# Kernel optimization log

Hardware: AMD Instinct MI355X
Metric: run time of the kernel (lower is better)

Reference implementation:

```python
import jax, jax.numpy as jnp
import numpy as np

B, S, H = 2, 2048, 2048
NQ, NKV = 32, 8          # query heads, kv heads
G = NQ // NKV            # query groups per kv head
D = H // NQ              # head dim = 64
MAX_POS = 4096
THETA = 10000.0


def _rope_tables(position_ids):
    # freqs per the original apply_rotary_emb (interleaved pair convention)
    freqs = 1.0 / THETA ** (jnp.arange(0, D, 2)[: D // 2].astype(jnp.float32) / D)
    t = jnp.arange(MAX_POS, dtype=jnp.float32)
    ang = jnp.outer(t, freqs)                     # [MAX_POS, D/2]
    cos = jnp.take(jnp.cos(ang), position_ids, axis=0)[:, :, None, :]  # [B,S,1,D/2]
    sin = jnp.take(jnp.sin(ang), position_ids, axis=0)[:, :, None, :]
    return cos, sin


def _apply_rope(x, cos, sin):
    # x: [B,S,h,D]; pairs are interleaved (x0,x1),(x2,x3),...
    x2 = x.astype(jnp.float32).reshape(*x.shape[:-1], D // 2, 2)
    xr, xi = x2[..., 0], x2[..., 1]
    out_r = xr * cos - xi * sin
    out_i = xr * sin + xi * cos
    return jnp.stack((out_r, out_i), axis=-1).reshape(x.shape).astype(x.dtype)


def setup_inputs() -> dict:
    key = jax.random.key(0)
    ks = jax.random.split(key, 5)
    init_scale = 0.02 / np.sqrt(H)
    hidden_states = jax.random.normal(ks[0], (B, S, H), dtype=jnp.float32)
    wq = jax.random.normal(ks[1], (H, H), dtype=jnp.float32) * init_scale
    wk = jax.random.normal(ks[2], (H, H // G), dtype=jnp.float32) * init_scale
    wv = jax.random.normal(ks[3], (H, H // G), dtype=jnp.float32) * init_scale
    wo = jax.random.normal(ks[4], (H, H), dtype=jnp.float32) * init_scale
    attention_mask = jnp.ones((B, S), dtype=jnp.int32)
    position_ids = jnp.broadcast_to(jnp.arange(S, dtype=jnp.int32), (B, S))
    return dict(hidden_states=hidden_states, attention_mask=attention_mask,
                position_ids=position_ids, wq=wq, wk=wk, wv=wv, wo=wo)


def reference(hidden_states, attention_mask, position_ids, wq, wk, wv, wo):
    # projections (no bias)
    xq = (hidden_states @ wq).reshape(B, S, NQ, D)
    xk = (hidden_states @ wk).reshape(B, S, NKV, D)
    xv = (hidden_states @ wv).reshape(B, S, NKV, D)
    # GQA repeat: kv head h -> query heads h*G .. h*G+G-1 (consecutive)
    xk = jnp.repeat(xk, G, axis=2)  # [B,S,NQ,D]
    xv = jnp.repeat(xv, G, axis=2)

    cos, sin = _rope_tables(position_ids)
    xq = _apply_rope(xq, cos, sin)
    xk = _apply_rope(xk, cos, sin)

    # causal + padding mask -> additive bias
    causal = jnp.tril(jnp.ones((S, S), dtype=bool))[None, None]          # [1,1,S,S]
    pad = (attention_mask > 0)[:, None, None, :]                          # [B,1,1,S]
    combined = jnp.logical_and(causal, pad)                               # [B,1,S,S]
    neg = jnp.finfo(jnp.float32).min
    bias = jnp.where(combined, 0.0, neg).astype(jnp.float32)

    scale = 1.0 / np.sqrt(D)
    scores = jnp.einsum('bqhd,bkhd->bhqk', xq, xk).astype(jnp.float32) * scale
    scores = scores + bias
    attn = jax.nn.softmax(scores, axis=-1)                                # [B,NQ,S,S] fp32
    out = jnp.einsum('bhqk,bkhd->bqhd', attn, xv)                         # [B,S,NQ,D]
    out = out.reshape(B, S, H)
    return out @ wo
```

## Files before the change

### kernel.cpp

```cpp
#include <hip/hip_runtime.h>
#include <cstdint>

typedef __attribute__((ext_vector_type(8))) __bf16  bf8v;
typedef __attribute__((ext_vector_type(4))) float   f4v;
typedef __attribute__((ext_vector_type(4))) short   s4v;
typedef __attribute__((ext_vector_type(8))) unsigned short ush8;

__device__ __forceinline__ float bf2f(unsigned short u) {
    union { unsigned u; float f; } v; v.u = ((unsigned)u) << 16; return v.f;
}
__device__ __forceinline__ unsigned short f2bf_n(float f) {
    union { __bf16 h; unsigned short s; } v; v.h = (__bf16)f; return v.s;
}
__device__ __forceinline__ unsigned pack2bf(float a, float b) {
    union { __bf16 h[2]; unsigned u; } v;
    v.h[0] = (__bf16)a; v.h[1] = (__bf16)b; return v.u;
}

#define GLDS16(gp, lp)                                                          \
    __builtin_amdgcn_global_load_lds(                                           \
        (const __attribute__((address_space(1))) void*)(uintptr_t)(gp),         \
        (__attribute__((address_space(3))) void*)(uintptr_t)(lp), 16, 0, 0)

__global__ void cast_f32_to_bf16(const float* __restrict__ in,
                                 unsigned short* __restrict__ out, int n8) {
    int i = blockIdx.x * 256 + threadIdx.x;
    if (i >= n8) return;
    float4 a = ((const float4*)in)[2 * i];
    float4 b = ((const float4*)in)[2 * i + 1];
    uint4 o;
    o.x = pack2bf(a.x, a.y);
    o.y = pack2bf(a.z, a.w);
    o.z = pack2bf(b.x, b.y);
    o.w = pack2bf(b.z, b.w);
    ((uint4*)out)[i] = o;
}

__global__ void transpose_cast(const float* __restrict__ in,
                               unsigned short* __restrict__ out, int R, int C) {
    __shared__ float t[32][33];
    int c0 = blockIdx.x * 32, r0 = blockIdx.y * 32;
    int x = threadIdx.x, y = threadIdx.y;
    #pragma unroll
    for (int i = 0; i < 32; i += 8) t[y + i][x] = in[(size_t)(r0 + y + i) * C + c0 + x];
    __syncthreads();
    #pragma unroll
    for (int i = 0; i < 32; i += 8)
        out[(size_t)(c0 + y + i) * R + r0 + x] = f2bf_n(t[x][y + i]);
}

__global__ void transpose_v_bf16(const unsigned short* __restrict__ in,
                                 unsigned short* __restrict__ out) {
    __shared__ unsigned short t[32][33];
    int c0 = blockIdx.x * 32;
    int r0 = blockIdx.y * 32;
    int x = threadIdx.x, y = threadIdx.y;
    #pragma unroll
    for (int i = 0; i < 32; i += 8)
        t[y + i][x] = in[(size_t)(r0 + y + i) * 3072 + 2560 + c0 + x];
    __syncthreads();
    #pragma unroll
    for (int i = 0; i < 32; i += 8) {
        int d   = c0 + y + i;
        int tok = r0 + x;
        int g   = (tok >> 2) & 15;
        int tp  = (tok & ~63) | (((g ^ (d & 15)) << 2)) | (tok & 3);
        out[(size_t)d * 4096 + tp] = t[x][y + i];
    }
}

__global__ void rope_strided(unsigned short* __restrict__ X,
                             const int* __restrict__ pos_ids,
                             int coloff, int stride, int nh_log2) {
    int idx = blockIdx.x * 256 + threadIdx.x;
    int i   = idx & 31;
    int hh  = (idx >> 5) & ((1 << nh_log2) - 1);
    int tok = idx >> (5 + nh_log2);
    int pos = pos_ids[tok];
    float ang = (float)pos * exp2f(-0.41524101186092f * (float)i);
    float s = sinf(ang), c = cosf(ang);
    unsigned short* p = X + (size_t)tok * stride + coloff + hh * 64 + 2 * i;
    unsigned pr = *(const unsigned*)p;
    float xr = bf2f((unsigned short)(pr & 0xffff));
    float xi = bf2f((unsigned short)(pr >> 16));
    float orr = xr * c - xi * s;
    float oi  = xr * s + xi * c;
    *(unsigned*)p = pack2bf(orr, oi);
}

template <int OUT_BF16>
__global__ __launch_bounds__(256) void gemm_bt(const unsigned short* __restrict__ A,
                                               const unsigned short* __restrict__ Bt,
                                               void* __restrict__ Cv, int N, int K) {
    __shared__ __align__(16) unsigned short As[128 * 64];
    __shared__ __align__(16) unsigned short Bs[128 * 64];
    const int t = threadIdx.x;
    const int lane = t & 63, w = t >> 6;
    const int wr = w >> 1, wc = w & 1;
    const int lr = lane & 15, lh = lane >> 4;
    const int m0 = blockIdx.y * 128, n0 = blockIdx.x * 128;

    f4v acc[4][4];
    #pragma unroll
    for (int i = 0; i < 4; ++i)
        #pragma unroll
        for (int j = 0; j < 4; ++j) acc[i][j] = f4v{0.f, 0.f, 0.f, 0.f};

    const int o_t = t * 16;
    for (int k0 = 0; k0 < K; k0 += 64) {
        __syncthreads();
        #pragma unroll
        for (int s = 0; s < 4; ++s) {
            int o = s * 4096 + o_t;
            int row = o >> 7;
            int src = (o & 127) ^ ((row & 7) << 4);
            const unsigned short* gA = A + (size_t)(m0 + row) * K + k0 + (src >> 1);
            GLDS16(gA, As + (o >> 1));
            const unsigned short* gB = Bt + (size_t)(n0 + row) * K + k0 + (src >> 1);
            GLDS16(gB, Bs + (o >> 1));
        }
        __syncthreads();
        #pragma unroll
        for (int kk = 0; kk < 2; ++kk) {
            bf8v af[4], bfr[4];
            #pragma unroll
            for (int mi = 0; mi < 4; ++mi) {
                int row = wr * 64 + mi * 16 + lr;
                int col = (kk * 32 + lh * 8) ^ ((row & 7) << 3);
                af[mi] = *(const bf8v*)(As + row * 64 + col);
            }
            #pragma unroll
            for (int ni = 0; ni < 4; ++ni) {
                int row = wc * 64 + ni * 16 + lr;
                int col = (kk * 32 + lh * 8) ^ ((row & 7) << 3);
                bfr[ni] = *(const bf8v*)(Bs + row * 64 + col);
            }
            #pragma unroll
            for (int mi = 0; mi < 4; ++mi)
                #pragma unroll
                for (int ni = 0; ni < 4; ++ni)
                    acc[mi][ni] = __builtin_amdgcn_mfma_f32_16x16x32_bf16(
                        af[mi], bfr[ni], acc[mi][ni], 0, 0, 0);
        }
    }
    #pragma unroll
    for (int mi = 0; mi < 4; ++mi)
        #pragma unroll
        for (int ni = 0; ni < 4; ++ni)
            #pragma unroll
            for (int r = 0; r < 4; ++r) {
                int row = m0 + wr * 64 + mi * 16 + lh * 4 + r;
                int col = n0 + wc * 64 + ni * 16 + lr;
                float v = acc[mi][ni][r];
                if (OUT_BF16) ((unsigned short*)Cv)[(size_t)row * N + col] = f2bf_n(v);
                else          ((float*)Cv)[(size_t)row * N + col] = v;
            }
}

__global__ __launch_bounds__(256, 4) void flash_attn(
        const unsigned short* __restrict__ QKV,
        const unsigned short* __restrict__ VtG,
        const int* __restrict__ amask,
        const int* __restrict__ pos_ids,
        unsigned short* __restrict__ O) {
    __shared__ __align__(16) unsigned short Ks[2][64 * 64];
    __shared__ __align__(16) unsigned short Vs[2][64 * 64];

    const int t = threadIdx.x, lane = t & 63, w = t >> 6;
    const int lr = lane & 15, lh = lane >> 4;
    const int pair = blockIdx.x, h = blockIdx.y, b = blockIdx.z;
    const size_t tok0 = (size_t)b * 2048;

    const unsigned short* Kb = QKV + tok0 * 3072 + 2048 + (h >> 2) * 64;
    const unsigned short* Vb = VtG + (size_t)((h >> 2) * 64) * 4096 + tok0;
    const int* amrow = amask + b * 2048;

#define STAGE(buf, kt)                                                              \
    {   _Pragma("unroll")                                                           \
        for (int s_ = 0; s_ < 2; ++s_) {                                            \
            int c_ = s_ * 256 + t;                                                  \
            int row_ = c_ >> 3;                                                     \
            int sc_ = (((c_ & 7) * 16) ^ ((row_ & 7) << 4)) >> 1;                   \
            GLDS16(Kb + (size_t)((kt) * 64 + row_) * 3072 + sc_, Ks[buf] + c_ * 8); \
            GLDS16(Vb + (size_t)row_ * 4096 + (kt) * 64 + (c_ & 7) * 8,             \
                   Vs[buf] + c_ * 8);                                               \
        }                                                                           \
    }

    const float SCL = 0.18033688011112042f;

    unsigned aliveMaskV = 0;
    {
        const int4* am4 = (const int4*)amrow;
        #pragma unroll
        for (int s = 0; s < 8; ++s) {
            int4 a = am4[s * 64 + lane];
            unsigned long long bal = __ballot(a.x && a.y && a.z && a.w);
            #pragma unroll
            for (int g = 0; g < 4; ++g)
                aliveMaskV |= (((bal >> (16 * g)) & 0xFFFFull) == 0xFFFFull)
                                  ? (1u << (4 * s + g)) : 0u;
        }
    }
    const int aliveMask = __builtin_amdgcn_readfirstlane((int)aliveMaskV);

    int vcol[4];
    #pragma unroll
    for (int kf = 0; kf < 4; ++kf) vcol[kf] = ((kf * 4 + lh) ^ lr) * 4;

    int cur = 0;

    #pragma unroll 1
    for (int half = 0; half < 2; ++half) {
        const int qt = half ? (31 - pair) : pair;
        const int q0 = qt * 64;
        const int nkv = qt + 1;
        const int qloc = w * 16 + lr;

        const unsigned short* Qp = QKV + (tok0 + q0 + qloc) * 3072 + h * 64;
        union Q8 { bf8v v; unsigned short s[8]; } qa0u, qa1u;
        qa0u.v = *(const bf8v*)(Qp + lh * 8);
        qa1u.v = *(const bf8v*)(Qp + 32 + lh * 8);
        {
            int pos = pos_ids[tok0 + q0 + qloc];
            #pragma unroll
            for (int r = 0; r < 4; ++r) {
                float i0 = (float)(lh * 4 + r);
                float ang0 = (float)pos * exp2f(-0.41524101186092f * i0);
                float sn = sinf(ang0), cs = cosf(ang0);
                float xr = bf2f(qa0u.s[2 * r]), xi = bf2f(qa0u.s[2 * r + 1]);
                qa0u.s[2 * r]     = f2bf_n((xr * cs - xi * sn) * SCL);
                qa0u.s[2 * r + 1] = f2bf_n((xr * sn + xi * cs) * SCL);
                float i1 = (float)(16 + lh * 4 + r);
                float ang1 = (float)pos * exp2f(-0.41524101186092f * i1);
                float sn1 = sinf(ang1), cs1 = cosf(ang1);
                float yr = bf2f(qa1u.s[2 * r]), yi = bf2f(qa1u.s[2 * r + 1]);
                qa1u.s[2 * r]     = f2bf_n((yr * cs1 - yi * sn1) * SCL);
                qa1u.s[2 * r + 1] = f2bf_n((yr * sn1 + yi * cs1) * SCL);
            }
        }
        const bf8v qa0 = qa0u.v, qa1 = qa1u.v;

        f4v oacc[4];
        #pragma unroll
        for (int i = 0; i < 4; ++i) oacc[i] = f4v{0.f, 0.f, 0.f, 0.f};
        float m_ = -1e30f, l_ = 0.f;

        STAGE(cur, 0);
        __syncthreads();

        #pragma unroll 1
        for (int kt = 0; kt < nkv; ++kt) {
            if (kt + 1 < nkv) STAGE(cur ^ 1, kt + 1);

            f4v sa[4];
            #pragma unroll
            for (int kf = 0; kf < 4; ++kf) sa[kf] = f4v{0.f, 0.f, 0.f, 0.f};
            __builtin_amdgcn_s_setprio(1);
            #pragma unroll
            for (int kk = 0; kk < 2; ++kk) {
                bf8v qa = kk ? qa1 : qa0;
                int col = kk * 32 + lh * 8;
                #pragma unroll
                for (int kf = 0; kf < 4; ++kf) {
                    bf8v kb = *(const bf8v*)(Ks[cur] + (kf * 16 + lr) * 64 + (col ^ ((lr & 7) << 3)));
                    sa[kf] = __builtin_amdgcn_mfma_f32_16x16x32_bf16(kb, qa, sa[kf], 0, 0, 0);
                }
            }
            __builtin_amdgcn_s_setprio(0);

            const bool diag = (kt == qt);
            const bool tileAlive = ((aliveMask >> kt) & 1) != 0;

            float pvv[4][4];
            if (tileAlive && !diag) {
                #pragma unroll
                for (int kf = 0; kf < 4; ++kf)
                    #pragma unroll
                    for (int r = 0; r < 4; ++r) pvv[kf][r] = sa[kf][r];
            } else if (tileAlive) {
                #pragma unroll
                for (int kf = 0; kf < 4; ++kf)
                    #pragma unroll
                    for (int r = 0; r < 4; ++r) {
                        int keyl = kf * 16 + lh * 4 + r;
                        pvv[kf][r] = (keyl > qloc) ? -1e30f : sa[kf][r];
                    }
            } else {
                int amv[4][4];
                #pragma unroll
                for (int kf = 0; kf < 4; ++kf) {
                    int4 aq = *(const int4*)(amrow + kt * 64 + kf * 16 + lh * 4);
                    amv[kf][0] = aq.x; amv[kf][1] = aq.y; amv[kf][2] = aq.z; amv[kf][3] = aq.w;
                }
                #pragma unroll
                for (int kf = 0; kf < 4; ++kf)
                    #pragma unroll
                    for (int r = 0; r < 4; ++r) {
                        int keyl = kf * 16 + lh * 4 + r;
                        bool dead = (amv[kf][r] == 0) || (diag && keyl > qloc);
                        pvv[kf][r] = dead ? -1e30f : sa[kf][r];
                    }
            }

            float t0 = fmaxf(fmaxf(pvv[0][0], pvv[0][1]), fmaxf(pvv[0][2], pvv[0][3]));
            float t1 = fmaxf(fmaxf(pvv[1][0], pvv[1][1]), fmaxf(pvv[1][2], pvv[1][3]));
            float t2 = fmaxf(fmaxf(pvv[2][0], pvv[2][1]), fmaxf(pvv[2][2], pvv[2][3]));
            float t3 = fmaxf(fmaxf(pvv[3][0], pvv[3][1]), fmaxf(pvv[3][2], pvv[3][3]));
            float mx = fmaxf(fmaxf(t0, t1), fmaxf(t2, t3));
            mx = fmaxf(mx, __shfl_xor(mx, 16));
            mx = fmaxf(mx, __shfl_xor(mx, 32));

            if (!__all(mx <= m_ + 8.0f)) {
                float mn = fmaxf(m_, mx);
                float fac = exp2f(m_ - mn);
                m_ = mn;
                l_ *= fac;
                float facr[4];
                #pragma unroll
                for (int r = 0; r < 4; ++r) facr[r] = __shfl(fac, lh * 4 + r);
                #pragma unroll
                for (int df = 0; df < 4; ++df) {
                    f4v o = oacc[df];
                    o[0] *= facr[0]; o[1] *= facr[1]; o[2] *= facr[2]; o[3] *= facr[3];
                    oacc[df] = o;
                }
            }

            float pe[4][4];
            #pragma unroll
            for (int kf = 0; kf < 4; ++kf)
                #pragma unroll
                for (int r = 0; r < 4; ++r)
                    pe[kf][r] = exp2f(pvv[kf][r] - m_);
            float s0 = (pe[0][0] + pe[0][1]) + (pe[0][2] + pe[0][3]);
            float s1 = (pe[1][0] + pe[1][1]) + (pe[1][2] + pe[1][3]);
            float s2 = (pe[2][0] + pe[2][1]) + (pe[2][2] + pe[2][3]);
            float s3 = (pe[3][0] + pe[3][1]) + (pe[3][2] + pe[3][3]);
            float rs = (s0 + s1) + (s2 + s3);
            rs += __shfl_xor(rs, 16);
            rs += __shfl_xor(rs, 32);
            l_ += rs;

            __builtin_amdgcn_s_setprio(1);
            #pragma unroll
            for (int kf = 0; kf < 4; ++kf) {
                union { uint2 u; s4v s; } pa;
                pa.u.x = pack2bf(pe[kf][0], pe[kf][1]);
                pa.u.y = pack2bf(pe[kf][2], pe[kf][3]);
                #pragma unroll
                for (int df = 0; df < 4; ++df) {
                    const s4v vb = *(const s4v*)(Vs[cur] + (df * 16 + lr) * 64 + vcol[kf]);
                    oacc[df] = __builtin_amdgcn_mfma_f32_16x16x16bf16_1k(
                        pa.s, vb, oacc[df], 0, 0, 0);
                }
            }
            __builtin_amdgcn_s_setprio(0);

            __syncthreads();
            cur ^= 1;
        }

        float invl = 1.0f / l_;
        float invr[4];
        #pragma unroll
        for (int r = 0; r < 4; ++r) invr[r] = __shfl(invl, lh * 4 + r);
        #pragma unroll
        for (int df = 0; df < 4; ++df)
            #pragma unroll
            for (int r = 0; r < 4; ++r) {
                int qg = q0 + w * 16 + lh * 4 + r;
                float v = oacc[df][r] * invr[r];
                O[(tok0 + qg) * 2048 + h * 64 + df * 16 + lr] = f2bf_n(v);
            }
    }
#undef STAGE
}

extern "C" void kernel_launch(void* const* d_in, const int* in_sizes, int n_in,
                              void* d_out, int out_size, void* d_ws, size_t ws_size,
                              hipStream_t stream) {
    const float* hs   = (const float*)d_in[0];
    const int* amask  = (const int*)d_in[1];
    const int* pos    = (const int*)d_in[2];
    const float* wq   = (const float*)d_in[3];
    const float* wk   = (const float*)d_in[4];
    const float* wv   = (const float*)d_in[5];
    const float* wo   = (const float*)d_in[6];

    char* ws = (char*)d_ws;
    unsigned short* Xb   = (unsigned short*)(ws);
    unsigned short* Wqkv = (unsigned short*)(ws + 16777216);
    unsigned short* Wot  = (unsigned short*)(ws + 29360128);
    unsigned short* AOb  = (unsigned short*)(ws + 37748736);

    char* ob = (char*)d_out;
    unsigned short* QKV = (unsigned short*)ob;
    unsigned short* VtG = (unsigned short*)(ob + 25165824);

    cast_f32_to_bf16<<<4096, 256, 0, stream>>>(hs, Xb, 1048576);
    transpose_cast<<<dim3(64, 64), dim3(32, 8), 0, stream>>>(wq, Wqkv, 2048, 2048);
    transpose_cast<<<dim3(16, 64), dim3(32, 8), 0, stream>>>(wk, Wqkv + 4194304, 2048, 512);
    transpose_cast<<<dim3(16, 64), dim3(32, 8), 0, stream>>>(wv, Wqkv + 5242880, 2048, 512);
    transpose_cast<<<dim3(64, 64), dim3(32, 8), 0, stream>>>(wo, Wot, 2048, 2048);

    gemm_bt<1><<<dim3(24, 32), 256, 0, stream>>>(Xb, Wqkv, (void*)QKV, 3072, 2048);

    rope_strided<<<4096, 256, 0, stream>>>(QKV, pos, 2048, 3072, 3);

    transpose_v_bf16<<<dim3(16, 128), dim3(32, 8), 0, stream>>>(QKV, VtG);

    flash_attn<<<dim3(16, 32, 2), 256, 0, stream>>>(QKV, VtG, amask, pos, AOb);

    gemm_bt<0><<<dim3(16, 32), 256, 0, stream>>>(AOb, Wot, d_out, 2048, 2048);
}
```

Before: 223.5 us.

## Peel diagonal tile, prefetch next half's first KV tile, use lazy-max softmax

New measurement: 225.4 us. No clear change (+0.8%).

```diff
diff --git a/kernel.cpp b/kernel.cpp
--- a/kernel.cpp
+++ b/kernel.cpp
@@ -3,6 +3,7 @@
 
 typedef __attribute__((ext_vector_type(8))) __bf16  bf8v;
 typedef __attribute__((ext_vector_type(4))) float   f4v;
+typedef __attribute__((ext_vector_type(2))) float   f2v;
 typedef __attribute__((ext_vector_type(4))) short   s4v;
 typedef __attribute__((ext_vector_type(8))) unsigned short ush8;
 
@@ -209,12 +210,12 @@
     for (int kf = 0; kf < 4; ++kf) vcol[kf] = ((kf * 4 + lh) ^ lr) * 4;
 
     int cur = 0;
+    STAGE(cur, 0);
 
     #pragma unroll 1
     for (int half = 0; half < 2; ++half) {
         const int qt = half ? (31 - pair) : pair;
         const int q0 = qt * 64;
-        const int nkv = qt + 1;
         const int qloc = w * 16 + lr;
 
         const unsigned short* Qp = QKV + (tok0 + q0 + qloc) * 3072 + h * 64;
@@ -245,15 +246,9 @@
         #pragma unroll
         for (int i = 0; i < 4; ++i) oacc[i] = f4v{0.f, 0.f, 0.f, 0.f};
         float m_ = -1e30f, l_ = 0.f;
-
-        STAGE(cur, 0);
-        __syncthreads();
-
-        #pragma unroll 1
-        for (int kt = 0; kt < nkv; ++kt) {
-            if (kt + 1 < nkv) STAGE(cur ^ 1, kt + 1);
-
-            f4v sa[4];
+        f4v sa[4];
+
+        auto qk = [&](int curb) {
             #pragma unroll
             for (int kf = 0; kf < 4; ++kf) sa[kf] = f4v{0.f, 0.f, 0.f, 0.f};
             __builtin_amdgcn_s_setprio(1);
@@ -263,55 +258,39 @@
                 int col = kk * 32 + lh * 8;
                 #pragma unroll
                 for (int kf = 0; kf < 4; ++kf) {
-                    bf8v kb = *(const bf8v*)(Ks[cur] + (kf * 16 + lr) * 64 + (col ^ ((lr & 7) << 3)));
+                    bf8v kb = *(const bf8v*)(Ks[curb] + (kf * 16 + lr) * 64 + (col ^ ((lr & 7) << 3)));
                     sa[kf] = __builtin_amdgcn_mfma_f32_16x16x32_bf16(kb, qa, sa[kf], 0, 0, 0);
                 }
             }
             __builtin_amdgcn_s_setprio(0);
-
-            const bool diag = (kt == qt);
-            const bool tileAlive = ((aliveMask >> kt) & 1) != 0;
-
-            float pvv[4][4];
-            if (tileAlive && !diag) {
+        };
+
+        auto softmax_pv = [&](int curb) {
+            float pe[4][4];
+            float rs;
+            #pragma unroll 1
+            for (;;) {
                 #pragma unroll
                 for (int kf = 0; kf < 4; ++kf)
                     #pragma unroll
-                    for (int r = 0; r < 4; ++r) pvv[kf][r] = sa[kf][r];
-            } else if (tileAlive) {
-                #pragma unroll
-                for (int kf = 0; kf < 4; ++kf)
-                    #pragma unroll
-                    for (int r = 0; r < 4; ++r) {
-                        int keyl = kf * 16 + lh * 4 + r;
-                        pvv[kf][r] = (keyl > qloc) ? -1e30f : sa[kf][r];
-                    }
-            } else {
-                int amv[4][4];
-                #pragma unroll
-                for (int kf = 0; kf < 4; ++kf) {
-                    int4 aq = *(const int4*)(amrow + kt * 64 + kf * 16 + lh * 4);
-                    amv[kf][0] = aq.x; amv[kf][1] = aq.y; amv[kf][2] = aq.z; amv[kf][3] = aq.w;
-                }
-                #pragma unroll
-                for (int kf = 0; kf < 4; ++kf)
-                    #pragma unroll
-                    for (int r = 0; r < 4; ++r) {
-                        int keyl = kf * 16 + lh * 4 + r;
-                        bool dead = (amv[kf][r] == 0) || (diag && keyl > qloc);
-                        pvv[kf][r] = dead ? -1e30f : sa[kf][r];
-                    }
-            }
-
-            float t0 = fmaxf(fmaxf(pvv[0][0], pvv[0][1]), fmaxf(pvv[0][2], pvv[0][3]));
-            float t1 = fmaxf(fmaxf(pvv[1][0], pvv[1][1]), fmaxf(pvv[1][2], pvv[1][3]));
-            float t2 = fmaxf(fmaxf(pvv[2][0], pvv[2][1]), fmaxf(pvv[2][2], pvv[2][3]));
-            float t3 = fmaxf(fmaxf(pvv[3][0], pvv[3][1]), fmaxf(pvv[3][2], pvv[3][3]));
-            float mx = fmaxf(fmaxf(t0, t1), fmaxf(t2, t3));
-            mx = fmaxf(mx, __shfl_xor(mx, 16));
-            mx = fmaxf(mx, __shfl_xor(mx, 32));
-
-            if (!__all(mx <= m_ + 8.0f)) {
+                    for (int r = 0; r < 4; ++r)
+                        pe[kf][r] = exp2f(sa[kf][r] - m_);
+                f2v v0 = f2v{pe[0][0], pe[0][1]} + f2v{pe[0][2], pe[0][3]};
+                f2v v1 = f2v{pe[1][0], pe[1][1]} + f2v{pe[1][2], pe[1][3]};
+                f2v v2 = f2v{pe[2][0], pe[2][1]} + f2v{pe[2][2], pe[2][3]};
+                f2v v3 = f2v{pe[3][0], pe[3][1]} + f2v{pe[3][2], pe[3][3]};
+                f2v vv = (v0 + v1) + (v2 + v3);
+                rs = vv[0] + vv[1];
+                rs += __shfl_xor(rs, 16);
+                rs += __shfl_xor(rs, 32);
+                if (__builtin_expect(!__any(rs > 16777216.0f), 1)) break;
+                float t0 = fmaxf(fmaxf(sa[0][0], sa[0][1]), fmaxf(sa[0][2], sa[0][3]));
+                float t1 = fmaxf(fmaxf(sa[1][0], sa[1][1]), fmaxf(sa[1][2], sa[1][3]));
+                float t2 = fmaxf(fmaxf(sa[2][0], sa[2][1]), fmaxf(sa[2][2], sa[2][3]));
+                float t3 = fmaxf(fmaxf(sa[3][0], sa[3][1]), fmaxf(sa[3][2], sa[3][3]));
+                float mx = fmaxf(fmaxf(t0, t1), fmaxf(t2, t3));
+                mx = fmaxf(mx, __shfl_xor(mx, 16));
+                mx = fmaxf(mx, __shfl_xor(mx, 32));
                 float mn = fmaxf(m_, mx);
                 float fac = exp2f(m_ - mn);
                 m_ = mn;
@@ -326,22 +305,7 @@
                     oacc[df] = o;
                 }
             }
-
-            float pe[4][4];
-            #pragma unroll
-            for (int kf = 0; kf < 4; ++kf)
-                #pragma unroll
-                for (int r = 0; r < 4; ++r)
-                    pe[kf][r] = exp2f(pvv[kf][r] - m_);
-            float s0 = (pe[0][0] + pe[0][1]) + (pe[0][2] + pe[0][3]);
-            float s1 = (pe[1][0] + pe[1][1]) + (pe[1][2] + pe[1][3]);
-            float s2 = (pe[2][0] + pe[2][1]) + (pe[2][2] + pe[2][3]);
-            float s3 = (pe[3][0] + pe[3][1]) + (pe[3][2] + pe[3][3]);
-            float rs = (s0 + s1) + (s2 + s3);
-            rs += __shfl_xor(rs, 16);
-            rs += __shfl_xor(rs, 32);
             l_ += rs;
-
             __builtin_amdgcn_s_setprio(1);
             #pragma unroll
             for (int kf = 0; kf < 4; ++kf) {
@@ -350,16 +314,63 @@
                 pa.u.y = pack2bf(pe[kf][2], pe[kf][3]);
                 #pragma unroll
                 for (int df = 0; df < 4; ++df) {
-                    const s4v vb = *(const s4v*)(Vs[cur] + (df * 16 + lr) * 64 + vcol[kf]);
+                    const s4v vb = *(const s4v*)(Vs[curb] + (df * 16 + lr) * 64 + vcol[kf]);
                     oacc[df] = __builtin_amdgcn_mfma_f32_16x16x16bf16_1k(
                         pa.s, vb, oacc[df], 0, 0, 0);
                 }
             }
             __builtin_amdgcn_s_setprio(0);
-
+        };
+
+        __syncthreads();
+
+        #pragma unroll 1
+        for (int kt = 0; kt < qt; ++kt) {
+            STAGE(cur ^ 1, kt + 1);
+            qk(cur);
+            if (!((aliveMask >> kt) & 1)) {
+                #pragma unroll
+                for (int kf = 0; kf < 4; ++kf) {
+                    int4 aq = *(const int4*)(amrow + kt * 64 + kf * 16 + lh * 4);
+                    if (aq.x == 0) sa[kf][0] = -1e30f;
+                    if (aq.y == 0) sa[kf][1] = -1e30f;
+                    if (aq.z == 0) sa[kf][2] = -1e30f;
+                    if (aq.w == 0) sa[kf][3] = -1e30f;
+                }
+            }
+            softmax_pv(cur);
             __syncthreads();
             cur ^= 1;
         }
+
+        if (half == 0) STAGE(cur ^ 1, 0);
+        qk(cur);
+        {
+            const bool tileAlive = ((aliveMask >> qt) & 1) != 0;
+            if (tileAlive) {
+                #pragma unroll
+                for (int kf = 0; kf < 4; ++kf)
+                    #pragma unroll
+                    for (int r = 0; r < 4; ++r) {
+                        int keyl = kf * 16 + lh * 4 + r;
+                        if (keyl > qloc) sa[kf][r] = -1e30f;
+                    }
+            } else {
+                #pragma unroll
+                for (int kf = 0; kf < 4; ++kf) {
+                    int4 aq = *(const int4*)(amrow + qt * 64 + kf * 16 + lh * 4);
+                    #pragma unroll
+                    for (int r = 0; r < 4; ++r) {
+                        int keyl = kf * 16 + lh * 4 + r;
+                        int am = r == 0 ? aq.x : r == 1 ? aq.y : r == 2 ? aq.z : aq.w;
+                        if (am == 0 || keyl > qloc) sa[kf][r] = -1e30f;
+                    }
+                }
+            }
+        }
+        softmax_pv(cur);
+        __syncthreads();
+        cur ^= 1;
 
         float invl = 1.0f / l_;
         float invr[4];
```
